# Optimization experiments

Hardware: AMD Instinct MI355X
Metric: run time of the kernel (lower is better)

The kernel has to match this reference:

```python
import jax, jax.numpy as jnp
import numpy as np
from jax import lax

B = 4_194_304  # batch rows
H = 7          # hidden width
N_MID = 19     # fc2..fc20


def setup_inputs() -> dict:
    key = jax.random.key(0)
    ks = jax.random.split(key, 7)
    x = jax.random.normal(ks[0], (B, 2), dtype=jnp.float32)
    # torch Linear default init scale ~ 1/sqrt(fan_in); use small uniform-like normals
    W1 = jax.random.normal(ks[1], (H, 2), dtype=jnp.float32) / jnp.sqrt(2.0)
    b1 = jax.random.normal(ks[2], (H,), dtype=jnp.float32) * 0.1
    Wm = jax.random.normal(ks[3], (N_MID, H, H), dtype=jnp.float32) / jnp.sqrt(float(H))
    bm = jax.random.normal(ks[4], (N_MID, H), dtype=jnp.float32) * 0.1
    Wo = jax.random.normal(ks[5], (2, H), dtype=jnp.float32) / jnp.sqrt(float(H))
    bo = jax.random.normal(ks[6], (2,), dtype=jnp.float32) * 0.1
    return {"x": x, "W1": W1, "b1": b1, "Wm": Wm, "bm": bm, "Wo": Wo, "bo": bo}


def reference(x, W1, b1, Wm, bm, Wo, bo):
    # fc1 + ELU
    h = jax.nn.elu(x @ W1.T + b1)  # [B, 7]

    # fc2..fc20 (19 identical-shape Linear(7,7)+ELU layers) via scan
    def step(h, wb):
        w, b = wb  # w: [7,7], b: [7]
        return jax.nn.elu(h @ w.T + b), None

    h, _ = lax.scan(step, h, (Wm, bm))

    # fc21 + log_softmax
    logits = h @ Wo.T + bo  # [B, 2]
    return jax.nn.log_softmax(logits, axis=1)
```

## Files before the change

kernel.cpp:

```cpp
#include <hip/hip_runtime.h>
#include <hip/hip_bf16.h>

#define HH 7
#define NMID 19

__global__ __launch_bounds__(256) void net_mlp_kernel(
    const float* __restrict__ x,
    const float* __restrict__ W1, const float* __restrict__ b1,
    const float* __restrict__ Wm, const float* __restrict__ bm,
    const float* __restrict__ Wo, const float* __restrict__ bo,
    float* __restrict__ out, int B)
{
    int i = blockIdx.x * blockDim.x + threadIdx.x;
    if (i >= B) return;

    const float2 xin = reinterpret_cast<const float2*>(x)[i];

    float h[HH];

#pragma unroll
    for (int j = 0; j < HH; ++j) {
        float a = fmaf(xin.x, W1[j * 2 + 0], fmaf(xin.y, W1[j * 2 + 1], b1[j]));
        h[j] = (a > 0.0f) ? a : (__expf(a) - 1.0f);
    }

#pragma unroll
    for (int l = 0; l < NMID; ++l) {
        const float* __restrict__ W = Wm + l * (HH * HH);
        const float* __restrict__ b = bm + l * HH;
        float nh[HH];
#pragma unroll
        for (int j = 0; j < HH; ++j) {
            float a = b[j];
#pragma unroll
            for (int k = 0; k < HH; ++k)
                a = fmaf(h[k], W[j * HH + k], a);
            nh[j] = (a > 0.0f) ? a : (__expf(a) - 1.0f);
        }
#pragma unroll
        for (int j = 0; j < HH; ++j) h[j] = nh[j];
    }

    float l0 = bo[0], l1 = bo[1];
#pragma unroll
    for (int k = 0; k < HH; ++k) {
        l0 = fmaf(h[k], Wo[k], l0);
        l1 = fmaf(h[k], Wo[HH + k], l1);
    }
    float m = fmaxf(l0, l1);
    float z = m + __logf(__expf(l0 - m) + __expf(l1 - m));

    float2 o;
    o.x = l0 - z;
    o.y = l1 - z;
    reinterpret_cast<float2*>(out)[i] = o;
}

extern "C" void kernel_launch(void* const* d_in, const int* in_sizes, int n_in,
                              void* d_out, int out_size, void* d_ws, size_t ws_size,
                              hipStream_t stream) {
    const float* x  = (const float*)d_in[0];
    const float* W1 = (const float*)d_in[1];
    const float* b1 = (const float*)d_in[2];
    const float* Wm = (const float*)d_in[3];
    const float* bm = (const float*)d_in[4];
    const float* Wo = (const float*)d_in[5];
    const float* bo = (const float*)d_in[6];
    float* out = (float*)d_out;

    const int B = in_sizes[0] / 2;
    const int block = 256;
    const int grid = (B + block - 1) / block;
    net_mlp_kernel<<<grid, block, 0, stream>>>(x, W1, b1, Wm, bm, Wo, bo, out, B);
}
```

Baseline: 238.0 us.

## Fold ELU offset into biases and use packed fp16 dot2 in log2 domain

Adds a prep kernel that rescales weights by log2(e), packs the mid and output weights into half2 pairs, and folds the ELU -1 offset into biases via row sums. The main kernel then computes each layer with fdot2 on packed fp16 activations and a single exp2 per neuron, plus a log2-domain log_softmax. This aims to cut the FMA and transcendental instruction count of a compute-bound per-row MLP. It trades fp32 accuracy for fp16 activations and weights, which risks tolerance failures, and adds a small extra launch.

Result: slower. 245.6 us (+3.2%).

```diff
diff --git a/kernel.cpp b/kernel.cpp
--- a/kernel.cpp
+++ b/kernel.cpp
@@ -1,58 +1,157 @@
 #include <hip/hip_runtime.h>
-#include <hip/hip_bf16.h>
 
-#define HH 7
 #define NMID 19
+#define LOG2E 1.4426950408889634f
+#define LN2   0.6931471805599453f
+
+typedef _Float16 h2 __attribute__((ext_vector_type(2)));
+
+__device__ __forceinline__ h2 uph(unsigned int u) {
+    return __builtin_bit_cast(h2, u);
+}
+
+__device__ __forceinline__ h2 pk(float a, float b) {
+    return __builtin_bit_cast(h2, __builtin_amdgcn_cvt_pkrtz(a, b));
+}
+
+__device__ __forceinline__ float exp2r(float x) {
+#if __has_builtin(__builtin_amdgcn_exp2f)
+    return __builtin_amdgcn_exp2f(x);
+#else
+    return __expf(x * LN2);
+#endif
+}
+
+__device__ __forceinline__ float log2r(float x) {
+#if __has_builtin(__builtin_amdgcn_logf)
+    return __builtin_amdgcn_logf(x);
+#else
+    return __logf(x) * LOG2E;
+#endif
+}
+
+__device__ __forceinline__ float fdot2(h2 a, h2 b, float c) {
+#if __has_builtin(__builtin_amdgcn_fdot2)
+    return __builtin_amdgcn_fdot2(a, b, c, false);
+#else
+    return fmaf((float)a[0], (float)b[0], fmaf((float)a[1], (float)b[1], c));
+#endif
+}
+
+__device__ __forceinline__ float elu1(float at) {
+    float e = exp2r(at);
+    float p = fmaf(at, LN2, 1.0f);
+    return (at > 0.0f) ? p : e;
+}
+
+#define NWORDS 696
+
+__device__ __forceinline__ unsigned int packh2(float a, float b) {
+    _Float16 ha = (_Float16)a, hb = (_Float16)b;
+    unsigned short ua = __builtin_bit_cast(unsigned short, ha);
+    unsigned short ub = __builtin_bit_cast(unsigned short, hb);
+    return (unsigned int)ua | ((unsigned int)ub << 16);
+}
+
+__global__ void prep_kernel(const float* __restrict__ W1, const float* __restrict__ b1,
+                            const float* __restrict__ Wm, const float* __restrict__ bm,
+                            const float* __restrict__ Wo, const float* __restrict__ bo,
+                            unsigned int* __restrict__ ws)
+{
+    for (int idx = threadIdx.x; idx < NWORDS; idx += blockDim.x) {
+        unsigned int uv;
+        if (idx < 14) {
+            uv = __float_as_uint(LOG2E * W1[idx]);
+        } else if (idx < 21) {
+            uv = __float_as_uint(LOG2E * b1[idx - 14]);
+        } else if (idx < 553) {
+            int q = idx - 21, l = q / 28, r = q % 28, j = r / 4, kk = r % 4;
+            const float* W = Wm + l * 49 + j * 7;
+            float a = LOG2E * W[kk * 2 + 0];
+            float b = (kk < 3) ? LOG2E * W[kk * 2 + 1] : 0.0f;
+            uv = packh2(a, b);
+        } else if (idx < 686) {
+            int q = idx - 553, l = q / 7, j = q % 7;
+            const float* W = Wm + l * 49 + j * 7;
+            float s = 0.0f;
+#pragma unroll
+            for (int k = 0; k < 7; ++k) s += W[k];
+            uv = __float_as_uint(LOG2E * (bm[l * 7 + j] - s));
+        } else if (idx < 694) {
+            int q = idx - 686, c = q / 4, kk = q % 4;
+            const float* W = Wo + c * 7;
+            float a = LOG2E * W[kk * 2 + 0];
+            float b = (kk < 3) ? LOG2E * W[kk * 2 + 1] : 0.0f;
+            uv = packh2(a, b);
+        } else {
+            int c = idx - 694;
+            const float* W = Wo + c * 7;
+            float s = 0.0f;
+#pragma unroll
+            for (int k = 0; k < 7; ++k) s += W[k];
+            uv = __float_as_uint(LOG2E * (bo[c] - s));
+        }
+        ws[idx] = uv;
+    }
+}
 
 __global__ __launch_bounds__(256) void net_mlp_kernel(
     const float* __restrict__ x,
-    const float* __restrict__ W1, const float* __restrict__ b1,
-    const float* __restrict__ Wm, const float* __restrict__ bm,
-    const float* __restrict__ Wo, const float* __restrict__ bo,
+    const unsigned int* __restrict__ ws,
     float* __restrict__ out, int B)
 {
     int i = blockIdx.x * blockDim.x + threadIdx.x;
     if (i >= B) return;
 
+    const float* wsf = reinterpret_cast<const float*>(ws);
     const float2 xin = reinterpret_cast<const float2*>(x)[i];
 
-    float h[HH];
-
+    float g[7];
 #pragma unroll
-    for (int j = 0; j < HH; ++j) {
-        float a = fmaf(xin.x, W1[j * 2 + 0], fmaf(xin.y, W1[j * 2 + 1], b1[j]));
-        h[j] = (a > 0.0f) ? a : (__expf(a) - 1.0f);
+    for (int j = 0; j < 7; ++j) {
+        float at = fmaf(xin.x, wsf[j * 2 + 0],
+                   fmaf(xin.y, wsf[j * 2 + 1], wsf[14 + j]));
+        g[j] = elu1(at);
     }
+    h2 gp0 = pk(g[0], g[1]);
+    h2 gp1 = pk(g[2], g[3]);
+    h2 gp2 = pk(g[4], g[5]);
+    h2 gp3 = pk(g[6], 0.0f);
 
 #pragma unroll
     for (int l = 0; l < NMID; ++l) {
-        const float* __restrict__ W = Wm + l * (HH * HH);
-        const float* __restrict__ b = bm + l * HH;
-        float nh[HH];
+        const unsigned int* wp = ws + 21 + l * 28;
+        const float* bt = wsf + 553 + l * 7;
+        float ng[7];
 #pragma unroll
-        for (int j = 0; j < HH; ++j) {
-            float a = b[j];
-#pragma unroll
-            for (int k = 0; k < HH; ++k)
-                a = fmaf(h[k], W[j * HH + k], a);
-            nh[j] = (a > 0.0f) ? a : (__expf(a) - 1.0f);
+        for (int j = 0; j < 7; ++j) {
+            float a = fdot2(gp0, uph(wp[j * 4 + 0]), bt[j]);
+            a       = fdot2(gp1, uph(wp[j * 4 + 1]), a);
+            a       = fdot2(gp2, uph(wp[j * 4 + 2]), a);
+            a       = fdot2(gp3, uph(wp[j * 4 + 3]), a);
+            ng[j] = elu1(a);
         }
-#pragma unroll
-        for (int j = 0; j < HH; ++j) h[j] = nh[j];
+        gp0 = pk(ng[0], ng[1]);
+        gp1 = pk(ng[2], ng[3]);
+        gp2 = pk(ng[4], ng[5]);
+        gp3 = pk(ng[6], 0.0f);
     }
 
-    float l0 = bo[0], l1 = bo[1];
-#pragma unroll
-    for (int k = 0; k < HH; ++k) {
-        l0 = fmaf(h[k], Wo[k], l0);
-        l1 = fmaf(h[k], Wo[HH + k], l1);
-    }
-    float m = fmaxf(l0, l1);
-    float z = m + __logf(__expf(l0 - m) + __expf(l1 - m));
+    float l0 = fdot2(gp0, uph(ws[686]), wsf[694]);
+    l0       = fdot2(gp1, uph(ws[687]), l0);
+    l0       = fdot2(gp2, uph(ws[688]), l0);
+    l0       = fdot2(gp3, uph(ws[689]), l0);
+    float l1 = fdot2(gp0, uph(ws[690]), wsf[695]);
+    l1       = fdot2(gp1, uph(ws[691]), l1);
+    l1       = fdot2(gp2, uph(ws[692]), l1);
+    l1       = fdot2(gp3, uph(ws[693]), l1);
 
+    float m  = fmaxf(l0, l1);
+    float d  = fminf(l0, l1) - m;
+    float zt = m + log2r(1.0f + exp2r(d));
     float2 o;
-    o.x = l0 - z;
-    o.y = l1 - z;
+    o.x = (l0 - zt) * LN2;
+    o.y = (l1 - zt) * LN2;
     reinterpret_cast<float2*>(out)[i] = o;
 }
 
@@ -67,9 +166,12 @@
     const float* Wo = (const float*)d_in[5];
     const float* bo = (const float*)d_in[6];
     float* out = (float*)d_out;
+    unsigned int* ws = (unsigned int*)d_ws;
+
+    prep_kernel<<<1, 256, 0, stream>>>(W1, b1, Wm, bm, Wo, bo, ws);
 
     const int B = in_sizes[0] / 2;
     const int block = 256;
     const int grid = (B + block - 1) / block;
-    net_mlp_kernel<<<grid, block, 0, stream>>>(x, W1, b1, Wm, bm, Wo, bo, out, B);
+    net_mlp_kernel<<<grid, block, 0, stream>>>(x, ws, out, B);
 }
```

## Run hidden layers in packed fp16 with branchless ELU and prescaled weights

Applied to the files above, without the earlier changes.

Adds a prep kernel that folds log2(e) scaling and a bias shift into the weights, storing the mid layers as replicated half2 values in the workspace. The main kernel then handles two rows per thread, running the 19 hidden layers with packed fp16 FMAs and a branchless exp2-based ELU, which roughly halves the ALU instruction count of this compute-bound kernel. The risk is fp16 precision loss over 19 layers, an extra kernel launch, and no tail handling when B is odd.

New measurement: 224.2 us. 1.06x faster.

```diff
diff --git a/kernel.cpp b/kernel.cpp
--- a/kernel.cpp
+++ b/kernel.cpp
@@ -1,59 +1,161 @@
 #include <hip/hip_runtime.h>
-#include <hip/hip_bf16.h>
+#include <hip/hip_fp16.h>
 
-#define HH 7
 #define NMID 19
+#define LOG2E 1.4426950408889634f
+#define LN2   0.6931471805599453f
+
+#define W1_OFF 0
+#define B1_OFF 14
+#define WM_OFF 21
+#define BM_OFF 952
+#define WO_OFF 1085
+#define BO_OFF 1099
+#define NWORDS 1101
+
+typedef _Float16 v2h __attribute__((ext_vector_type(2)));
+
+__device__ __forceinline__ float exp2r(float x) {
+#if __has_builtin(__builtin_amdgcn_exp2f)
+    return __builtin_amdgcn_exp2f(x);
+#else
+    return __expf(x * LN2);
+#endif
+}
+__device__ __forceinline__ float log2r(float x) {
+#if __has_builtin(__builtin_amdgcn_logf)
+    return __builtin_amdgcn_logf(x);
+#else
+    return __logf(x) * LOG2E;
+#endif
+}
+
+__device__ __forceinline__ __half2 pmin2(__half2 a, __half2 b) {
+    v2h av = __builtin_bit_cast(v2h, a), bv = __builtin_bit_cast(v2h, b);
+    return __builtin_bit_cast(__half2, __builtin_elementwise_min(av, bv));
+}
+__device__ __forceinline__ __half2 pmax2(__half2 a, __half2 b) {
+    v2h av = __builtin_bit_cast(v2h, a), bv = __builtin_bit_cast(v2h, b);
+    return __builtin_bit_cast(__half2, __builtin_elementwise_max(av, bv));
+}
+
+__device__ __forceinline__ unsigned int reph(float v) {
+    _Float16 h = (_Float16)v;
+    unsigned short u = __builtin_bit_cast(unsigned short, h);
+    return (unsigned int)u * 0x00010001u;
+}
+
+__global__ void prep_kernel(const float* __restrict__ W1, const float* __restrict__ b1,
+                            const float* __restrict__ Wm, const float* __restrict__ bm,
+                            const float* __restrict__ Wo, const float* __restrict__ bo,
+                            unsigned int* __restrict__ ws)
+{
+    for (int idx = threadIdx.x; idx < NWORDS; idx += blockDim.x) {
+        unsigned int uv;
+        if (idx < B1_OFF) {
+            uv = __float_as_uint(LOG2E * W1[idx]);
+        } else if (idx < WM_OFF) {
+            uv = __float_as_uint(LOG2E * b1[idx - B1_OFF]);
+        } else if (idx < BM_OFF) {
+            int q = idx - WM_OFF;
+            uv = reph(LOG2E * Wm[q]);
+        } else if (idx < WO_OFF) {
+            int q = idx - BM_OFF, l = q / 7, j = q % 7;
+            const float* W = Wm + l * 49 + j * 7;
+            float s = 0.0f;
+#pragma unroll
+            for (int k = 0; k < 7; ++k) s += W[k];
+            uv = reph(LOG2E * (bm[l * 7 + j] - s));
+        } else if (idx < BO_OFF) {
+            int q = idx - WO_OFF;
+            uv = __float_as_uint(LOG2E * Wo[q]);
+        } else {
+            int c = idx - BO_OFF;
+            const float* W = Wo + c * 7;
+            float s = 0.0f;
+#pragma unroll
+            for (int k = 0; k < 7; ++k) s += W[k];
+            uv = __float_as_uint(LOG2E * (bo[c] - s));
+        }
+        ws[idx] = uv;
+    }
+}
+
+__device__ __forceinline__ __half2 pelu(__half2 at, __half2 ln22, __half2 one2) {
+    __half2 E = h2exp2(at);
+    __half2 P = __hfma2(at, ln22, one2);
+    return __hmul2(pmin2(E, one2), pmax2(P, one2));
+}
 
 __global__ __launch_bounds__(256) void net_mlp_kernel(
     const float* __restrict__ x,
-    const float* __restrict__ W1, const float* __restrict__ b1,
-    const float* __restrict__ Wm, const float* __restrict__ bm,
-    const float* __restrict__ Wo, const float* __restrict__ bo,
+    const unsigned int* __restrict__ ws,
     float* __restrict__ out, int B)
 {
     int i = blockIdx.x * blockDim.x + threadIdx.x;
-    if (i >= B) return;
+    if (2 * i >= B) return;
 
-    const float2 xin = reinterpret_cast<const float2*>(x)[i];
+    const float* wsf = reinterpret_cast<const float*>(ws);
+    const __half2* wsh = reinterpret_cast<const __half2*>(ws);
 
-    float h[HH];
+    const float4 xx = reinterpret_cast<const float4*>(x)[i];
 
+    const __half2 one2 = __float2half2_rn(1.0f);
+    const __half2 ln22 = __float2half2_rn(LN2);
+
+    __half2 g[7];
 #pragma unroll
-    for (int j = 0; j < HH; ++j) {
-        float a = fmaf(xin.x, W1[j * 2 + 0], fmaf(xin.y, W1[j * 2 + 1], b1[j]));
-        h[j] = (a > 0.0f) ? a : (__expf(a) - 1.0f);
+    for (int j = 0; j < 7; ++j) {
+        float w0 = wsf[W1_OFF + 2 * j], w1 = wsf[W1_OFF + 2 * j + 1], bb = wsf[B1_OFF + j];
+        float aA = fmaf(xx.x, w0, fmaf(xx.y, w1, bb));
+        float aB = fmaf(xx.z, w0, fmaf(xx.w, w1, bb));
+        g[j] = pelu(__floats2half2_rn(aA, aB), ln22, one2);
     }
 
 #pragma unroll
     for (int l = 0; l < NMID; ++l) {
-        const float* __restrict__ W = Wm + l * (HH * HH);
-        const float* __restrict__ b = bm + l * HH;
-        float nh[HH];
+        const __half2* wp = wsh + WM_OFF + l * 49;
+        const __half2* bp = wsh + BM_OFF + l * 7;
+        __half2 ng[7];
 #pragma unroll
-        for (int j = 0; j < HH; ++j) {
-            float a = b[j];
+        for (int j = 0; j < 7; ++j) {
+            __half2 acc = bp[j];
 #pragma unroll
-            for (int k = 0; k < HH; ++k)
-                a = fmaf(h[k], W[j * HH + k], a);
-            nh[j] = (a > 0.0f) ? a : (__expf(a) - 1.0f);
+            for (int k = 0; k < 7; ++k)
+                acc = __hfma2(g[k], wp[j * 7 + k], acc);
+            ng[j] = pelu(acc, ln22, one2);
         }
 #pragma unroll
-        for (int j = 0; j < HH; ++j) h[j] = nh[j];
+        for (int j = 0; j < 7; ++j) g[j] = ng[j];
     }
 
-    float l0 = bo[0], l1 = bo[1];
+    float l0A = wsf[BO_OFF + 0], l1A = wsf[BO_OFF + 1];
+    float l0B = l0A, l1B = l1A;
 #pragma unroll
-    for (int k = 0; k < HH; ++k) {
-        l0 = fmaf(h[k], Wo[k], l0);
-        l1 = fmaf(h[k], Wo[HH + k], l1);
+    for (int k = 0; k < 7; ++k) {
+        float gA = __low2float(g[k]);
+        float gB = __high2float(g[k]);
+        float w0 = wsf[WO_OFF + k], w1 = wsf[WO_OFF + 7 + k];
+        l0A = fmaf(gA, w0, l0A);
+        l1A = fmaf(gA, w1, l1A);
+        l0B = fmaf(gB, w0, l0B);
+        l1B = fmaf(gB, w1, l1B);
     }
-    float m = fmaxf(l0, l1);
-    float z = m + __logf(__expf(l0 - m) + __expf(l1 - m));
 
-    float2 o;
-    o.x = l0 - z;
-    o.y = l1 - z;
-    reinterpret_cast<float2*>(out)[i] = o;
+    float4 o;
+    {
+        float m = fmaxf(l0A, l1A), d = fminf(l0A, l1A) - m;
+        float zt = m + log2r(1.0f + exp2r(d));
+        o.x = (l0A - zt) * LN2;
+        o.y = (l1A - zt) * LN2;
+    }
+    {
+        float m = fmaxf(l0B, l1B), d = fminf(l0B, l1B) - m;
+        float zt = m + log2r(1.0f + exp2r(d));
+        o.z = (l0B - zt) * LN2;
+        o.w = (l1B - zt) * LN2;
+    }
+    reinterpret_cast<float4*>(out)[i] = o;
 }
 
 extern "C" void kernel_launch(void* const* d_in, const int* in_sizes, int n_in,
@@ -67,9 +169,13 @@
     const float* Wo = (const float*)d_in[5];
     const float* bo = (const float*)d_in[6];
     float* out = (float*)d_out;
+    unsigned int* ws = (unsigned int*)d_ws;
+
+    prep_kernel<<<1, 256, 0, stream>>>(W1, b1, Wm, bm, Wo, bo, ws);
 
     const int B = in_sizes[0] / 2;
+    const int pairs = (B + 1) / 2;
     const int block = 256;
-    const int grid = (B + block - 1) / block;
-    net_mlp_kernel<<<grid, block, 0, stream>>>(x, W1, b1, Wm, bm, Wo, bo, out, B);
+    const int grid = (pairs + block - 1) / block;
+    net_mlp_kernel<<<grid, block, 0, stream>>>(x, ws, out, B);
 }
```
